# Optimization experiments

Hardware: AMD Instinct MI355X
Metric: run time of the kernel (lower is better)

The kernel has to match this reference:

```python
import jax, jax.numpy as jnp
import numpy as np

N_NODES = 100000
N_EDGES = 1200000
IN_FEATS = 64
H_FEATS = 128
NUM_CLASSES = 32


def setup_inputs() -> dict:
    key = jax.random.key(0)
    ks = jax.random.split(key, 8)
    in_feat = jax.random.normal(ks[0], (N_NODES, IN_FEATS), dtype=jnp.float32)
    src = jax.random.randint(ks[1], (N_EDGES,), 0, N_NODES, dtype=jnp.int64)
    dst = jax.random.randint(ks[2], (N_EDGES,), 0, N_NODES, dtype=jnp.int64)
    edge_weight = jax.random.uniform(ks[3], (N_EDGES,), dtype=jnp.float32)
    W1 = jax.random.normal(ks[4], (H_FEATS, IN_FEATS), dtype=jnp.float32) * (1.0 / np.sqrt(IN_FEATS))
    b1 = jax.random.normal(ks[5], (H_FEATS,), dtype=jnp.float32) * 0.01
    W2 = jax.random.normal(ks[6], (NUM_CLASSES, H_FEATS), dtype=jnp.float32) * (1.0 / np.sqrt(H_FEATS))
    b2 = jax.random.normal(ks[7], (NUM_CLASSES,), dtype=jnp.float32) * 0.01
    return {"in_feat": in_feat, "src": src, "dst": dst, "edge_weight": edge_weight,
            "W1": W1, "b1": b1, "W2": W2, "b2": b2}


def _gin_conv_max(x, src, dst, edge_weight, W, b):
    # DGL GINConv('max') with eps=0: linear(x_dst + max_{e: src->dst}(x_src * w_e))
    msg = x[src] * edge_weight[:, None]                     # [E, F] gather + scale
    agg = jax.ops.segment_max(msg, dst, num_segments=N_NODES)  # [N, F]
    # empty segments are filled with -inf (dtype min); DGL yields 0 there
    agg = jnp.where(jnp.isfinite(agg), agg, jnp.zeros_like(agg))
    return (x + agg) @ W.T + b


def reference(in_feat, src, dst, edge_weight, W1, b1, W2, b2):
    h = _gin_conv_max(in_feat, src, dst, edge_weight, W1, b1)
    h = jax.nn.relu(h)
    h = _gin_conv_max(h, src, dst, edge_weight, W2, b2)
    return h
```

## Files before the change

### kernel.cpp

```cpp
#include <hip/hip_runtime.h>
#include <stdint.h>

typedef unsigned short ushort_t;

static constexpr int N_NODES = 100000;
static constexpr int N_EDGES = 1200000;
static constexpr int IN_FEATS = 64;
static constexpr int H_FEATS = 128;
static constexpr int NUM_CLASSES = 32;
static constexpr int CHUNK = 4096;
static constexpr int NBUCK = (N_NODES + 1023) / 1024;
static constexpr int CAP = 14336;

__device__ __forceinline__ ushort_t f2bf(float f) {
    unsigned u = __float_as_uint(f);
    return (ushort_t)((u + 0x7fffu + ((u >> 16) & 1u)) >> 16);
}
__device__ __forceinline__ float bf2f(ushort_t u) {
    return __uint_as_float((unsigned)u << 16);
}

__device__ __forceinline__ unsigned enc_rec(int s, float w) {
    unsigned u = __float_as_uint(w);
    int E5 = (int)((u >> 23) & 0xff) - 101;
    unsigned code = (E5 < 1) ? 0u : (((unsigned)E5 << 10) | ((u >> 13) & 0x3ffu));
    return ((unsigned)s << 15) | code;
}
__device__ __forceinline__ float rec_w(unsigned r) {
    return __uint_as_float(((((r >> 10) & 31u) + 101u) << 23) | ((r & 1023u) << 13));
}

__device__ __forceinline__ float tree16(const float* v) {
    float t0 = fmaxf(fmaxf(fmaxf(v[0], v[1]), fmaxf(v[2], v[3])),
                     fmaxf(fmaxf(v[4], v[5]), fmaxf(v[6], v[7])));
    float t1 = fmaxf(fmaxf(fmaxf(v[8], v[9]), fmaxf(v[10], v[11])),
                     fmaxf(fmaxf(v[12], v[13]), fmaxf(v[14], v[15])));
    return fmaxf(t0, t1);
}

__device__ __forceinline__ void unp8(uint4 u, float* f) {
    f[0] = __uint_as_float(u.x << 16); f[1] = __uint_as_float(u.x & 0xFFFF0000u);
    f[2] = __uint_as_float(u.y << 16); f[3] = __uint_as_float(u.y & 0xFFFF0000u);
    f[4] = __uint_as_float(u.z << 16); f[5] = __uint_as_float(u.z & 0xFFFF0000u);
    f[6] = __uint_as_float(u.w << 16); f[7] = __uint_as_float(u.w & 0xFFFF0000u);
}

__global__ __launch_bounds__(256) void to_bf16(const float4* __restrict__ in,
                                               ushort4* __restrict__ out, int n4) {
    int i = blockIdx.x * 256 + threadIdx.x;
    if (i < n4) {
        float4 v = in[i];
        ushort4 o;
        o.x = f2bf(v.x); o.y = f2bf(v.y); o.z = f2bf(v.z); o.w = f2bf(v.w);
        out[i] = o;
    }
}

__global__ __launch_bounds__(128) void init_bcur(int* __restrict__ bcur) {
    if (threadIdx.x < NBUCK) bcur[threadIdx.x] = threadIdx.x * CAP;
}

__global__ __launch_bounds__(256) void passA_bin(const int* __restrict__ src,
                                                 const int* __restrict__ dst,
                                                 const float* __restrict__ w,
                                                 int* __restrict__ bcur,
                                                 uint2* __restrict__ pairs_g) {
    __shared__ int cnt[256];
    __shared__ int off[256];
    __shared__ int off2[256];
    __shared__ int gbase[128];
    __shared__ uint2 stage[CHUNK];
    const int t = threadIdx.x;
    const int base = blockIdx.x * CHUNK;
    const int nch = min(CHUNK, N_EDGES - base);

    cnt[t] = 0;
    __syncthreads();

    unsigned rec_r[16];
    int dst_r[16];
#pragma unroll
    for (int k = 0; k < 16; ++k) {
        int e = base + k * 256 + t;
        if (e < N_EDGES) {
            int d = dst[e];
            dst_r[k] = d;
            rec_r[k] = enc_rec(src[e], w[e]);
            atomicAdd(&cnt[d >> 10], 1);
        } else {
            dst_r[k] = -1;
        }
    }
    __syncthreads();

    int v = cnt[t];
    off[t] = v;
    __syncthreads();
    for (int d = 1; d < 256; d <<= 1) {
        int x = (t >= d) ? off[t - d] : 0;
        __syncthreads();
        off[t] += x;
        __syncthreads();
    }
    int excl = off[t] - v;
    __syncthreads();
    off[t] = excl;
    off2[t] = excl;
    if (t < NBUCK) gbase[t] = atomicAdd(&bcur[t], cnt[t]);
    __syncthreads();

#pragma unroll
    for (int k = 0; k < 16; ++k) {
        if (dst_r[k] >= 0) {
            int b = dst_r[k] >> 10;
            int slot = atomicAdd(&off2[b], 1);
            stage[slot] = make_uint2(rec_r[k], (unsigned)dst_r[k]);
        }
    }
    __syncthreads();

    for (int s = t; s < nch; s += 256) {
        uint2 pr = stage[s];
        int b = (int)(pr.y >> 10);
        int g = gbase[b] + (s - off[b]);
        pairs_g[g] = pr;
    }
}

__global__ __launch_bounds__(256) void passB_place(const uint2* __restrict__ pairs_g,
                                                   const int* __restrict__ bcur,
                                                   int2* __restrict__ rp2,
                                                   unsigned* __restrict__ ed) {
    __shared__ int lcnt[1024];
    __shared__ int tsum[256];
    const int b = blockIdx.x, t = threadIdx.x;
    const int lo = b * CAP;
    const int hi = bcur[b];
    const int n0 = b << 10;
    const int nlim = min(1024, N_NODES - n0);

    for (int i = t; i < 1024; i += 256) lcnt[i] = 0;
    __syncthreads();
    for (int p = lo + t; p < hi; p += 256)
        atomicAdd(&lcnt[pairs_g[p].y & 1023], 1);
    __syncthreads();

    int a0 = lcnt[t * 4], a1 = lcnt[t * 4 + 1], a2 = lcnt[t * 4 + 2], a3 = lcnt[t * 4 + 3];
    int ms = a0 + a1 + a2 + a3;
    tsum[t] = ms;
    __syncthreads();
    for (int d = 1; d < 256; d <<= 1) {
        int x = (t >= d) ? tsum[t - d] : 0;
        __syncthreads();
        tsum[t] += x;
        __syncthreads();
    }
    int tb = tsum[t] - ms;
    lcnt[t * 4]     = tb;
    lcnt[t * 4 + 1] = tb + a0;
    lcnt[t * 4 + 2] = tb + a0 + a1;
    lcnt[t * 4 + 3] = tb + a0 + a1 + a2;
    {
        int i0 = t * 4;
        int st[4] = {tb, tb + a0, tb + a0 + a1, tb + a0 + a1 + a2};
        int ct[4] = {a0, a1, a2, a3};
#pragma unroll
        for (int j = 0; j < 4; ++j)
            if (i0 + j < nlim)
                rp2[n0 + i0 + j] = make_int2(lo + st[j], lo + st[j] + ct[j]);
    }
    __syncthreads();

    for (int p = lo + t; p < hi; p += 256) {
        uint2 pr = pairs_g[p];
        int pos = lo + atomicAdd(&lcnt[pr.y & 1023], 1);
        ed[pos] = pr.x;
    }
}

template <int F, bool RESID>
__global__ __launch_bounds__(256) void reduce_max(const ushort_t* __restrict__ xg,
                                                  const unsigned* __restrict__ ed,
                                                  const int2* __restrict__ rp2,
                                                  ushort_t* __restrict__ obf) {
    constexpr int VPT = F / 64;
    const int t = threadIdx.x;
    const int p = t >> 6;
    const int lane = t & 63;
    const int c = lane * VPT;
    const int n = blockIdx.x * 4 + p;
    const int2 se = rp2[n];
    const int s = __builtin_amdgcn_readfirstlane(se.x);
    const int e = __builtin_amdgcn_readfirstlane(se.y);

    float m0 = -INFINITY, m1 = -INFINITY;

    for (int s0 = s; s0 < e; s0 += 64) {
        const int tile = min(64, e - s0);
        unsigned myrec = ed[s0 + lane];
        for (int k = 0; k < tile; k += 16) {
            float v0[16], v1[16];
#pragma unroll
            for (int kk = 0; kk < 16; ++kk) {
                int ki = min(k + kk, tile - 1);
                unsigned rr = (unsigned)__builtin_amdgcn_readlane((int)myrec, ki);
                float wk = rec_w(rr);
                const ushort_t* row = xg + (size_t)(rr >> 15) * F;
                if (VPT == 1) {
                    v0[kk] = bf2f(row[c]) * wk;
                } else {
                    ushort2 u = *(const ushort2*)&row[c];
                    v0[kk] = bf2f(u.x) * wk;
                    v1[kk] = bf2f(u.y) * wk;
                }
            }
            m0 = fmaxf(m0, tree16(v0));
            if (VPT == 2) m1 = fmaxf(m1, tree16(v1));
        }
    }

    if (m0 == -INFINITY) m0 = 0.0f;
    if (m1 == -INFINITY) m1 = 0.0f;

    const size_t base = (size_t)n * F + c;
    if (RESID) {
        if (VPT == 1) {
            obf[base] = f2bf(bf2f(xg[base]) + m0);
        } else {
            ushort2 xv = *(const ushort2*)&xg[base];
            ushort2 o;
            o.x = f2bf(bf2f(xv.x) + m0);
            o.y = f2bf(bf2f(xv.y) + m1);
            *(ushort2*)&obf[base] = o;
        }
    } else {
        if (VPT == 1) {
            obf[base] = f2bf(m0);
        } else {
            ushort2 o;
            o.x = f2bf(m0);
            o.y = f2bf(m1);
            *(ushort2*)&obf[base] = o;
        }
    }
}

template <int FIN, int FOUT, int TNL, int KC, bool RELU, bool OUTF32>
__global__ __launch_bounds__(256) void gin_gemm(const ushort_t* __restrict__ xa,
                                                const float* __restrict__ W,
                                                const float* __restrict__ b,
                                                float* __restrict__ outf,
                                                ushort_t* __restrict__ outb) {
    constexpr int NX = FOUT / 8;
    constexpr int NY = 256 / NX;
    constexpr int TM = NY * TNL;
    __shared__ float xs[KC][TM + 4];
    __shared__ float ws_[KC][FOUT + 4];
    const int t = threadIdx.x;
    const int nx = t % NX, ny = t / NX;
    const int of0 = nx * 8, nl0 = ny * TNL;
    const long long n0 = (long long)blockIdx.x * TM;

    float acc[TNL][8];
    {
        float4 b0 = *(const float4*)&b[of0];
        float4 b1 = *(const float4*)&b[of0 + 4];
#pragma unroll
        for (int i = 0; i < TNL; ++i) {
            acc[i][0] = b0.x; acc[i][1] = b0.y; acc[i][2] = b0.z; acc[i][3] = b0.w;
            acc[i][4] = b1.x; acc[i][5] = b1.y; acc[i][6] = b1.z; acc[i][7] = b1.w;
        }
    }

    for (int kc = 0; kc < FIN; kc += KC) {
        for (int idx = t; idx < TM * KC / 8; idx += 256) {
            int nl = idx / (KC / 8), kq = idx % (KC / 8);
            long long n = n0 + nl;
            float f[8] = {0.f, 0.f, 0.f, 0.f, 0.f, 0.f, 0.f, 0.f};
            if (n < N_NODES) {
                uint4 u = *(const uint4*)(xa + n * FIN + kc + kq * 8);
                unp8(u, f);
            }
#pragma unroll
            for (int q = 0; q < 8; ++q) xs[kq * 8 + q][nl] = f[q];
        }
        for (int idx = t; idx < FOUT * KC / 4; idx += 256) {
            int of = idx / (KC / 4), kq = idx % (KC / 4);
            float4 v = *((const float4*)(W + of * FIN + kc) + kq);
            ws_[kq * 4 + 0][of] = v.x;
            ws_[kq * 4 + 1][of] = v.y;
            ws_[kq * 4 + 2][of] = v.z;
            ws_[kq * 4 + 3][of] = v.w;
        }
        __syncthreads();
#pragma unroll 4
        for (int k = 0; k < KC; ++k) {
            float a[TNL];
#pragma unroll
            for (int i = 0; i < TNL; i += 4) {
                float4 av = *(const float4*)&xs[k][nl0 + i];
                a[i] = av.x; a[i + 1] = av.y; a[i + 2] = av.z; a[i + 3] = av.w;
            }
            float4 w0 = *(float4*)&ws_[k][of0];
            float4 w1 = *(float4*)&ws_[k][of0 + 4];
#pragma unroll
            for (int i = 0; i < TNL; ++i) {
                acc[i][0] = fmaf(a[i], w0.x, acc[i][0]);
                acc[i][1] = fmaf(a[i], w0.y, acc[i][1]);
                acc[i][2] = fmaf(a[i], w0.z, acc[i][2]);
                acc[i][3] = fmaf(a[i], w0.w, acc[i][3]);
                acc[i][4] = fmaf(a[i], w1.x, acc[i][4]);
                acc[i][5] = fmaf(a[i], w1.y, acc[i][5]);
                acc[i][6] = fmaf(a[i], w1.z, acc[i][6]);
                acc[i][7] = fmaf(a[i], w1.w, acc[i][7]);
            }
        }
        __syncthreads();
    }

#pragma unroll
    for (int i = 0; i < TNL; ++i) {
        long long n = n0 + nl0 + i;
        if (n < N_NODES) {
            float o[8];
#pragma unroll
            for (int q = 0; q < 8; ++q)
                o[q] = RELU ? fmaxf(acc[i][q], 0.f) : acc[i][q];
            if (OUTF32) {
                *(float4*)&outf[n * FOUT + of0] =
                    make_float4(o[0], o[1], o[2], o[3]);
                *(float4*)&outf[n * FOUT + of0 + 4] =
                    make_float4(o[4], o[5], o[6], o[7]);
            } else {
                uint4 u;
                u.x = (unsigned)f2bf(o[0]) | ((unsigned)f2bf(o[1]) << 16);
                u.y = (unsigned)f2bf(o[2]) | ((unsigned)f2bf(o[3]) << 16);
                u.z = (unsigned)f2bf(o[4]) | ((unsigned)f2bf(o[5]) << 16);
                u.w = (unsigned)f2bf(o[6]) | ((unsigned)f2bf(o[7]) << 16);
                *(uint4*)&outb[n * FOUT + of0] = u;
            }
        }
    }
}

extern "C" void kernel_launch(void* const* d_in, const int* in_sizes, int n_in,
                              void* d_out, int out_size, void* d_ws, size_t ws_size,
                              hipStream_t stream) {
    const float* x   = (const float*)d_in[0];
    const int*   src = (const int*)d_in[1];
    const int*   dst = (const int*)d_in[2];
    const float* w   = (const float*)d_in[3];
    const float* W1  = (const float*)d_in[4];
    const float* b1  = (const float*)d_in[5];
    const float* W2  = (const float*)d_in[6];
    const float* b2  = (const float*)d_in[7];
    float* out = (float*)d_out;

    char* wsb = (char*)d_ws;
    uint2*    pairs = (uint2*)wsb;
    ushort_t* xa1   = (ushort_t*)wsb;
    ushort_t* xa2   = (ushort_t*)(wsb + 12800000);
    ushort_t* xbf   = (ushort_t*)(wsb + 38400000);
    ushort_t* hbf   = (ushort_t*)(wsb + 51200000);

    char* ob = (char*)d_out;
    unsigned* ed   = (unsigned*)ob;
    int2*     rp2  = (int2*)(ob + 5620000);
    int*      bcur = (int*)(ob + 6420000);

    const int AB = (N_EDGES + CHUNK - 1) / CHUNK;

    to_bf16<<<(N_NODES * IN_FEATS / 4) / 256, 256, 0, stream>>>(
        (const float4*)x, (ushort4*)xbf, N_NODES * IN_FEATS / 4);

    init_bcur<<<1, 128, 0, stream>>>(bcur);
    passA_bin<<<AB, 256, 0, stream>>>(src, dst, w, bcur, pairs);
    passB_place<<<NBUCK, 256, 0, stream>>>(pairs, bcur, rp2, ed);

    reduce_max<IN_FEATS, true><<<N_NODES / 4, 256, 0, stream>>>(xbf, ed, rp2, xa1);
    gin_gemm<IN_FEATS, H_FEATS, 8, 64, true, false>
        <<<(N_NODES + 127) / 128, 256, 0, stream>>>(xa1, W1, b1, nullptr, hbf);

    reduce_max<H_FEATS, true><<<N_NODES / 4, 256, 0, stream>>>(hbf, ed, rp2, xa2);
    gin_gemm<H_FEATS, NUM_CLASSES, 4, 64, false, true>
        <<<(N_NODES + 255) / 256, 256, 0, stream>>>(xa2, W2, b2, out, nullptr);
}
```

Before: 197.0 us.

## Fuse max-aggregation with GEMM per layer and fold bucket init into conversion

Each GIN layer now runs as one kernel. Each block aggregates 128 nodes into a bf16 shared tile (one wave per 32 nodes) and then multiplies that tile against W staged in shared memory. This removes the intermediate aggregated-feature buffer and its global write and re-read, plus two launches. The separate bucket-init kernel is merged into the bf16 conversion kernel. The cost is far fewer blocks and waves doing the latency-bound gather, with larger shared memory per block, so less latency hiding.

```diff
diff --git a/kernel.cpp b/kernel.cpp
--- a/kernel.cpp
+++ b/kernel.cpp
@@ -38,26 +38,17 @@
     return fmaxf(t0, t1);
 }
 
-__device__ __forceinline__ void unp8(uint4 u, float* f) {
-    f[0] = __uint_as_float(u.x << 16); f[1] = __uint_as_float(u.x & 0xFFFF0000u);
-    f[2] = __uint_as_float(u.y << 16); f[3] = __uint_as_float(u.y & 0xFFFF0000u);
-    f[4] = __uint_as_float(u.z << 16); f[5] = __uint_as_float(u.z & 0xFFFF0000u);
-    f[6] = __uint_as_float(u.w << 16); f[7] = __uint_as_float(u.w & 0xFFFF0000u);
-}
-
 __global__ __launch_bounds__(256) void to_bf16(const float4* __restrict__ in,
-                                               ushort4* __restrict__ out, int n4) {
+                                               ushort4* __restrict__ out, int n4,
+                                               int* __restrict__ bcur) {
     int i = blockIdx.x * 256 + threadIdx.x;
+    if (blockIdx.x == 0 && threadIdx.x < NBUCK) bcur[threadIdx.x] = threadIdx.x * CAP;
     if (i < n4) {
         float4 v = in[i];
         ushort4 o;
         o.x = f2bf(v.x); o.y = f2bf(v.y); o.z = f2bf(v.z); o.w = f2bf(v.w);
         out[i] = o;
     }
-}
-
-__global__ __launch_bounds__(128) void init_bcur(int* __restrict__ bcur) {
-    if (threadIdx.x < NBUCK) bcur[threadIdx.x] = threadIdx.x * CAP;
 }
 
 __global__ __launch_bounds__(256) void passA_bin(const int* __restrict__ src,
@@ -178,89 +169,88 @@
     }
 }
 
-template <int F, bool RESID>
-__global__ __launch_bounds__(256) void reduce_max(const ushort_t* __restrict__ xg,
-                                                  const unsigned* __restrict__ ed,
-                                                  const int2* __restrict__ rp2,
-                                                  ushort_t* __restrict__ obf) {
-    constexpr int VPT = F / 64;
+template <int FIN, int FOUT, bool RELU, bool OUTF32>
+__global__ __launch_bounds__(256) void fused_layer(
+    const ushort_t* __restrict__ xg,
+    const unsigned* __restrict__ ed,
+    const int2* __restrict__ rp2,
+    const float* __restrict__ W,
+    const float* __restrict__ b,
+    float* __restrict__ outf,
+    ushort_t* __restrict__ outb) {
+    constexpr int VPT = FIN / 64;
+    constexpr int TM = 128;
+    constexpr int PAD = 8;
+    constexpr int NX = FOUT / 8;
+    constexpr int NY = 256 / NX;
+    constexpr int TNL = TM / NY;
+    __shared__ ushort_t xsb[FIN][TM + PAD];
+    __shared__ float ws_[FIN][FOUT + 4];
     const int t = threadIdx.x;
-    const int p = t >> 6;
-    const int lane = t & 63;
-    const int c = lane * VPT;
-    const int n = blockIdx.x * 4 + p;
-    const int2 se = rp2[n];
-    const int s = __builtin_amdgcn_readfirstlane(se.x);
-    const int e = __builtin_amdgcn_readfirstlane(se.y);
-
-    float m0 = -INFINITY, m1 = -INFINITY;
-
-    for (int s0 = s; s0 < e; s0 += 64) {
-        const int tile = min(64, e - s0);
-        unsigned myrec = ed[s0 + lane];
-        for (int k = 0; k < tile; k += 16) {
-            float v0[16], v1[16];
-#pragma unroll
-            for (int kk = 0; kk < 16; ++kk) {
-                int ki = min(k + kk, tile - 1);
-                unsigned rr = (unsigned)__builtin_amdgcn_readlane((int)myrec, ki);
-                float wk = rec_w(rr);
-                const ushort_t* row = xg + (size_t)(rr >> 15) * F;
+    const long long n0 = (long long)blockIdx.x * TM;
+
+    for (int idx = t; idx < FOUT * FIN / 4; idx += 256) {
+        int of = idx / (FIN / 4), kq = idx % (FIN / 4);
+        float4 v = *((const float4*)(W + of * FIN) + kq);
+        ws_[kq * 4 + 0][of] = v.x;
+        ws_[kq * 4 + 1][of] = v.y;
+        ws_[kq * 4 + 2][of] = v.z;
+        ws_[kq * 4 + 3][of] = v.w;
+    }
+
+    {
+        const int wv = t >> 6, lane = t & 63;
+        const int c = lane * VPT;
+        for (int q = 0; q < 32; ++q) {
+            const int nl = wv * 32 + q;
+            const long long n = n0 + nl;
+            float xa0 = 0.f, xa1 = 0.f;
+            if (n < N_NODES) {
+                const int2 se = rp2[n];
+                const int s = __builtin_amdgcn_readfirstlane(se.x);
+                const int e = __builtin_amdgcn_readfirstlane(se.y);
+                float m0 = -INFINITY, m1 = -INFINITY;
+                for (int s0 = s; s0 < e; s0 += 64) {
+                    const int tile = min(64, e - s0);
+                    unsigned myrec = ed[s0 + lane];
+                    for (int k = 0; k < tile; k += 16) {
+                        float v0[16], v1[16];
+#pragma unroll
+                        for (int kk = 0; kk < 16; ++kk) {
+                            int ki = min(k + kk, tile - 1);
+                            unsigned rr = (unsigned)__builtin_amdgcn_readlane((int)myrec, ki);
+                            float wk = rec_w(rr);
+                            const ushort_t* row = xg + (size_t)(rr >> 15) * FIN;
+                            if (VPT == 1) {
+                                v0[kk] = bf2f(row[c]) * wk;
+                            } else {
+                                ushort2 u = *(const ushort2*)&row[c];
+                                v0[kk] = bf2f(u.x) * wk;
+                                v1[kk] = bf2f(u.y) * wk;
+                            }
+                        }
+                        m0 = fmaxf(m0, tree16(v0));
+                        if (VPT == 2) m1 = fmaxf(m1, tree16(v1));
+                    }
+                }
+                if (m0 == -INFINITY) m0 = 0.0f;
+                if (m1 == -INFINITY) m1 = 0.0f;
                 if (VPT == 1) {
-                    v0[kk] = bf2f(row[c]) * wk;
+                    xa0 = bf2f(xg[(size_t)n * FIN + c]) + m0;
                 } else {
-                    ushort2 u = *(const ushort2*)&row[c];
-                    v0[kk] = bf2f(u.x) * wk;
-                    v1[kk] = bf2f(u.y) * wk;
+                    ushort2 xv = *(const ushort2*)&xg[(size_t)n * FIN + c];
+                    xa0 = bf2f(xv.x) + m0;
+                    xa1 = bf2f(xv.y) + m1;
                 }
             }
-            m0 = fmaxf(m0, tree16(v0));
-            if (VPT == 2) m1 = fmaxf(m1, tree16(v1));
-        }
-    }
-
-    if (m0 == -INFINITY) m0 = 0.0f;
-    if (m1 == -INFINITY) m1 = 0.0f;
-
-    const size_t base = (size_t)n * F + c;
-    if (RESID) {
-        if (VPT == 1) {
-            obf[base] = f2bf(bf2f(xg[base]) + m0);
-        } else {
-            ushort2 xv = *(const ushort2*)&xg[base];
-            ushort2 o;
-            o.x = f2bf(bf2f(xv.x) + m0);
-            o.y = f2bf(bf2f(xv.y) + m1);
-            *(ushort2*)&obf[base] = o;
-        }
-    } else {
-        if (VPT == 1) {
-            obf[base] = f2bf(m0);
-        } else {
-            ushort2 o;
-            o.x = f2bf(m0);
-            o.y = f2bf(m1);
-            *(ushort2*)&obf[base] = o;
-        }
-    }
-}
-
-template <int FIN, int FOUT, int TNL, int KC, bool RELU, bool OUTF32>
-__global__ __launch_bounds__(256) void gin_gemm(const ushort_t* __restrict__ xa,
-                                                const float* __restrict__ W,
-                                                const float* __restrict__ b,
-                                                float* __restrict__ outf,
-                                                ushort_t* __restrict__ outb) {
-    constexpr int NX = FOUT / 8;
-    constexpr int NY = 256 / NX;
-    constexpr int TM = NY * TNL;
-    __shared__ float xs[KC][TM + 4];
-    __shared__ float ws_[KC][FOUT + 4];
-    const int t = threadIdx.x;
+            xsb[c][nl] = f2bf(xa0);
+            if (VPT == 2) xsb[c + 1][nl] = f2bf(xa1);
+        }
+    }
+    __syncthreads();
+
     const int nx = t % NX, ny = t / NX;
     const int of0 = nx * 8, nl0 = ny * TNL;
-    const long long n0 = (long long)blockIdx.x * TM;
-
     float acc[TNL][8];
     {
         float4 b0 = *(const float4*)&b[of0];
@@ -271,51 +261,33 @@
             acc[i][4] = b1.x; acc[i][5] = b1.y; acc[i][6] = b1.z; acc[i][7] = b1.w;
         }
     }
-
-    for (int kc = 0; kc < FIN; kc += KC) {
-        for (int idx = t; idx < TM * KC / 8; idx += 256) {
-            int nl = idx / (KC / 8), kq = idx % (KC / 8);
-            long long n = n0 + nl;
-            float f[8] = {0.f, 0.f, 0.f, 0.f, 0.f, 0.f, 0.f, 0.f};
-            if (n < N_NODES) {
-                uint4 u = *(const uint4*)(xa + n * FIN + kc + kq * 8);
-                unp8(u, f);
-            }
-#pragma unroll
-            for (int q = 0; q < 8; ++q) xs[kq * 8 + q][nl] = f[q];
-        }
-        for (int idx = t; idx < FOUT * KC / 4; idx += 256) {
-            int of = idx / (KC / 4), kq = idx % (KC / 4);
-            float4 v = *((const float4*)(W + of * FIN + kc) + kq);
-            ws_[kq * 4 + 0][of] = v.x;
-            ws_[kq * 4 + 1][of] = v.y;
-            ws_[kq * 4 + 2][of] = v.z;
-            ws_[kq * 4 + 3][of] = v.w;
-        }
-        __syncthreads();
 #pragma unroll 4
-        for (int k = 0; k < KC; ++k) {
-            float a[TNL];
-#pragma unroll
-            for (int i = 0; i < TNL; i += 4) {
-                float4 av = *(const float4*)&xs[k][nl0 + i];
-                a[i] = av.x; a[i + 1] = av.y; a[i + 2] = av.z; a[i + 3] = av.w;
-            }
-            float4 w0 = *(float4*)&ws_[k][of0];
-            float4 w1 = *(float4*)&ws_[k][of0 + 4];
-#pragma unroll
-            for (int i = 0; i < TNL; ++i) {
-                acc[i][0] = fmaf(a[i], w0.x, acc[i][0]);
-                acc[i][1] = fmaf(a[i], w0.y, acc[i][1]);
-                acc[i][2] = fmaf(a[i], w0.z, acc[i][2]);
-                acc[i][3] = fmaf(a[i], w0.w, acc[i][3]);
-                acc[i][4] = fmaf(a[i], w1.x, acc[i][4]);
-                acc[i][5] = fmaf(a[i], w1.y, acc[i][5]);
-                acc[i][6] = fmaf(a[i], w1.z, acc[i][6]);
-                acc[i][7] = fmaf(a[i], w1.w, acc[i][7]);
-            }
-        }
-        __syncthreads();
+    for (int k = 0; k < FIN; ++k) {
+        float a[TNL];
+        if (TNL == 8) {
+            uint4 u = *(const uint4*)&xsb[k][nl0];
+            a[0] = __uint_as_float(u.x << 16); a[1] = __uint_as_float(u.x & 0xFFFF0000u);
+            a[2] = __uint_as_float(u.y << 16); a[3] = __uint_as_float(u.y & 0xFFFF0000u);
+            a[4] = __uint_as_float(u.z << 16); a[5] = __uint_as_float(u.z & 0xFFFF0000u);
+            a[6] = __uint_as_float(u.w << 16); a[7] = __uint_as_float(u.w & 0xFFFF0000u);
+        } else {
+            unsigned u = *(const unsigned*)&xsb[k][nl0];
+            a[0] = __uint_as_float(u << 16);
+            if (TNL > 1) a[1] = __uint_as_float(u & 0xFFFF0000u);
+        }
+        float4 w0 = *(float4*)&ws_[k][of0];
+        float4 w1 = *(float4*)&ws_[k][of0 + 4];
+#pragma unroll
+        for (int i = 0; i < TNL; ++i) {
+            acc[i][0] = fmaf(a[i], w0.x, acc[i][0]);
+            acc[i][1] = fmaf(a[i], w0.y, acc[i][1]);
+            acc[i][2] = fmaf(a[i], w0.z, acc[i][2]);
+            acc[i][3] = fmaf(a[i], w0.w, acc[i][3]);
+            acc[i][4] = fmaf(a[i], w1.x, acc[i][4]);
+            acc[i][5] = fmaf(a[i], w1.y, acc[i][5]);
+            acc[i][6] = fmaf(a[i], w1.z, acc[i][6]);
+            acc[i][7] = fmaf(a[i], w1.w, acc[i][7]);
+        }
     }
 
 #pragma unroll
@@ -327,10 +299,8 @@
             for (int q = 0; q < 8; ++q)
                 o[q] = RELU ? fmaxf(acc[i][q], 0.f) : acc[i][q];
             if (OUTF32) {
-                *(float4*)&outf[n * FOUT + of0] =
-                    make_float4(o[0], o[1], o[2], o[3]);
-                *(float4*)&outf[n * FOUT + of0 + 4] =
-                    make_float4(o[4], o[5], o[6], o[7]);
+                *(float4*)&outf[n * FOUT + of0] = make_float4(o[0], o[1], o[2], o[3]);
+                *(float4*)&outf[n * FOUT + of0 + 4] = make_float4(o[4], o[5], o[6], o[7]);
             } else {
                 uint4 u;
                 u.x = (unsigned)f2bf(o[0]) | ((unsigned)f2bf(o[1]) << 16);
@@ -358,30 +328,24 @@
 
     char* wsb = (char*)d_ws;
     uint2*    pairs = (uint2*)wsb;
-    ushort_t* xa1   = (ushort_t*)wsb;
-    ushort_t* xa2   = (ushort_t*)(wsb + 12800000);
-    ushort_t* xbf   = (ushort_t*)(wsb + 38400000);
-    ushort_t* hbf   = (ushort_t*)(wsb + 51200000);
-
-    char* ob = (char*)d_out;
-    unsigned* ed   = (unsigned*)ob;
-    int2*     rp2  = (int2*)(ob + 5620000);
-    int*      bcur = (int*)(ob + 6420000);
+    unsigned* ed    = (unsigned*)(wsb + 11500000);
+    int2*     rp2   = (int2*)(wsb + 17500000);
+    int*      bcur  = (int*)(wsb + 18500000);
+    ushort_t* xbf   = (ushort_t*)(wsb + 20000000);
+    ushort_t* hbf   = (ushort_t*)(wsb + 33000000);
 
     const int AB = (N_EDGES + CHUNK - 1) / CHUNK;
+    const int FB = (N_NODES + 127) / 128;
 
     to_bf16<<<(N_NODES * IN_FEATS / 4) / 256, 256, 0, stream>>>(
-        (const float4*)x, (ushort4*)xbf, N_NODES * IN_FEATS / 4);
-
-    init_bcur<<<1, 128, 0, stream>>>(bcur);
+        (const float4*)x, (ushort4*)xbf, N_NODES * IN_FEATS / 4, bcur);
+
     passA_bin<<<AB, 256, 0, stream>>>(src, dst, w, bcur, pairs);
     passB_place<<<NBUCK, 256, 0, stream>>>(pairs, bcur, rp2, ed);
 
-    reduce_max<IN_FEATS, true><<<N_NODES / 4, 256, 0, stream>>>(xbf, ed, rp2, xa1);
-    gin_gemm<IN_FEATS, H_FEATS, 8, 64, true, false>
-        <<<(N_NODES + 127) / 128, 256, 0, stream>>>(xa1, W1, b1, nullptr, hbf);
-
-    reduce_max<H_FEATS, true><<<N_NODES / 4, 256, 0, stream>>>(hbf, ed, rp2, xa2);
-    gin_gemm<H_FEATS, NUM_CLASSES, 4, 64, false, true>
-        <<<(N_NODES + 255) / 256, 256, 0, stream>>>(xa2, W2, b2, out, nullptr);
-}
+    fused_layer<IN_FEATS, H_FEATS, true, false>
+        <<<FB, 256, 0, stream>>>(xbf, ed, rp2, W1, b1, nullptr, hbf);
+
+    fused_layer<H_FEATS, NUM_CLASSES, false, true>
+        <<<FB, 256, 0, stream>>>(hbf, ed, rp2, W2, b2, out, nullptr);
+}
```

Result: slower. 311.3 us (+58.0%).
